# Performance work log

Measured on AMD Instinct MI355X. Metric: run time of the kernel, lower is better.

## Reference

```python
import jax, jax.numpy as jnp
import numpy as np

B, T, F_CGM, F_OTH = 128, 288, 16, 64
U, H = 256, 4
HD = U // H  # head dim 64
EPS = 1e-6
NBLK = 2


def layer_norm(x, s, b):
    m = jnp.mean(x, axis=-1, keepdims=True)
    v = jnp.mean(jnp.square(x - m), axis=-1, keepdims=True)
    return (x - m) * jax.lax.rsqrt(v + EPS) * s + b


def gru(x, Wi, bi, Wh, bhn):
    # flax GRUCell math (deterministic / no dropout):
    # r = sigmoid(W_ir x + b_ir + W_hr h); z = sigmoid(W_iz x + b_iz + W_hz h)
    # n = tanh(W_in x + b_in + r * (W_hn h + b_hn)); h' = (1-z)*n + z*h
    xg = jnp.einsum('btf,fg->btg', x, Wi) + bi  # [B,T,3U], precomputed input gates
    h0 = jnp.zeros((x.shape[0], U), x.dtype)

    def step(h, xg_t):
        hg = h @ Wh  # [B,3U]
        r = jax.nn.sigmoid(xg_t[:, :U] + hg[:, :U])
        z = jax.nn.sigmoid(xg_t[:, U:2 * U] + hg[:, U:2 * U])
        n = jnp.tanh(xg_t[:, 2 * U:] + r * (hg[:, 2 * U:] + bhn))
        h_new = (1.0 - z) * n + z * h
        return h_new, h_new

    _, ys = jax.lax.scan(step, h0, xg.transpose(1, 0, 2))  # time-major scan
    return ys.transpose(1, 0, 2)  # [B,T,U]


def mha(x, Wq, bq, Wk, bk, Wv, bv, Wo, bo):
    b, t, _ = x.shape
    q = (x @ Wq + bq).reshape(b, t, H, HD)
    k = (x @ Wk + bk).reshape(b, t, H, HD)
    v = (x @ Wv + bv).reshape(b, t, H, HD)
    scores = jnp.einsum('bqhd,bkhd->bhqk', q, k) / jnp.sqrt(jnp.asarray(HD, x.dtype))
    p = jax.nn.softmax(scores, axis=-1)
    o = jnp.einsum('bhqk,bkhd->bqhd', p, v).reshape(b, t, U)
    return o @ Wo + bo


def forward(cgm, other, d0_W, d0_b, ln0_s, ln0_b,
            gru_Wi, gru_bi, gru_Wh, gru_bhn, ln1_s, ln1_b,
            Wq, bq, Wk, bk, Wv, bv, Wo, bo, ln2_s, ln2_b,
            m1_W, m1_b, lm1_s, lm1_b, m2_W, m2_b, lm2_s, lm2_b,
            out_W, out_b):
    x = cgm @ d0_W + d0_b                      # [B,T,U]
    x = layer_norm(x, ln0_s, ln0_b)
    for i in range(NBLK):
        skip1 = x
        g = gru(x, gru_Wi[i], gru_bi[i], gru_Wh[i], gru_bhn[i])
        g = layer_norm(g, ln1_s[i], ln1_b[i])
        x = g + skip1                          # dims always match (U == U)
        skip2 = x
        a = mha(x, Wq[i], bq[i], Wk[i], bk[i], Wv[i], bv[i], Wo[i], bo[i])
        x = layer_norm(a + skip2, ln2_s[i], ln2_b[i])
    x = jnp.mean(x, axis=1)                    # [B,U]
    c = jnp.concatenate([x, other], axis=-1)   # [B,U+F_OTH]
    # MLP head; residual branches never match (320->128, 128->64), so no skips
    h1 = layer_norm(jax.nn.relu(c @ m1_W + m1_b), lm1_s, lm1_b)
    h2 = layer_norm(jax.nn.relu(h1 @ m2_W + m2_b), lm2_s, lm2_b)
    return h2 @ out_W + out_b                  # [B,1]


def setup_inputs() -> dict:
    key = jax.random.key(0)
    ks = jax.random.split(key, 16)
    f32 = jnp.float32
    rn = lambda k, shp, s: jax.random.normal(k, shp, dtype=f32) * s
    return {
        'cgm': jax.random.normal(ks[0], (B, T, F_CGM), dtype=f32),
        'other': jax.random.normal(ks[1], (B, F_OTH), dtype=f32),
        'd0_W': rn(ks[2], (F_CGM, U), 0.1), 'd0_b': jnp.zeros((U,), f32),
        'ln0_s': jnp.ones((U,), f32), 'ln0_b': jnp.zeros((U,), f32),
        'gru_Wi': rn(ks[3], (NBLK, U, 3 * U), 0.05), 'gru_bi': jnp.zeros((NBLK, 3 * U), f32),
        'gru_Wh': rn(ks[4], (NBLK, U, 3 * U), 0.05), 'gru_bhn': jnp.zeros((NBLK, U), f32),
        'ln1_s': jnp.ones((NBLK, U), f32), 'ln1_b': jnp.zeros((NBLK, U), f32),
        'Wq': rn(ks[5], (NBLK, U, U), 0.05), 'bq': jnp.zeros((NBLK, U), f32),
        'Wk': rn(ks[6], (NBLK, U, U), 0.05), 'bk': jnp.zeros((NBLK, U), f32),
        'Wv': rn(ks[7], (NBLK, U, U), 0.05), 'bv': jnp.zeros((NBLK, U), f32),
        'Wo': rn(ks[8], (NBLK, U, U), 0.05), 'bo': jnp.zeros((NBLK, U), f32),
        'ln2_s': jnp.ones((NBLK, U), f32), 'ln2_b': jnp.zeros((NBLK, U), f32),
        'm1_W': rn(ks[9], (U + F_OTH, 128), 0.05), 'm1_b': jnp.zeros((128,), f32),
        'lm1_s': jnp.ones((128,), f32), 'lm1_b': jnp.zeros((128,), f32),
        'm2_W': rn(ks[10], (128, 64), 0.05), 'm2_b': jnp.zeros((64,), f32),
        'lm2_s': jnp.ones((64,), f32), 'lm2_b': jnp.zeros((64,), f32),
        'out_W': rn(ks[11], (64, 1), 0.05), 'out_b': jnp.zeros((1,), f32),
    }


def reference(cgm, other, d0_W, d0_b, ln0_s, ln0_b,
              gru_Wi, gru_bi, gru_Wh, gru_bhn, ln1_s, ln1_b,
              Wq, bq, Wk, bk, Wv, bv, Wo, bo, ln2_s, ln2_b,
              m1_W, m1_b, lm1_s, lm1_b, m2_W, m2_b, lm2_s, lm2_b,
              out_W, out_b):
    return forward(cgm, other, d0_W, d0_b, ln0_s, ln0_b,
                   gru_Wi, gru_bi, gru_Wh, gru_bhn, ln1_s, ln1_b,
                   Wq, bq, Wk, bk, Wv, bv, Wo, bo, ln2_s, ln2_b,
                   m1_W, m1_b, lm1_s, lm1_b, m2_W, m2_b, lm2_s, lm2_b,
                   out_W, out_b)
```

## Files before the change

kernel.cpp:

```cpp
#include <hip/hip_runtime.h>
#include <math.h>

#define B_   128
#define T_   288
#define U_   256
#define H_   4
#define HD_  64
#define MT   (B_*T_)
#define EPSF 1e-6f

typedef _Float16 h2_t  __attribute__((ext_vector_type(2)));
typedef _Float16 f16x4 __attribute__((ext_vector_type(4)));
typedef _Float16 f16x8 __attribute__((ext_vector_type(8)));
typedef float    f32x4 __attribute__((ext_vector_type(4)));

#if defined(__has_builtin)
#  if __has_builtin(__builtin_amdgcn_fdot2)
#    define HAS_FDOT2 1
#  endif
#endif
#ifndef HAS_FDOT2
#  define HAS_FDOT2 0
#endif

template<bool TB>
__global__ __launch_bounds__(256) void gemm_kernel(
    const float* __restrict__ A, const float* __restrict__ Bm,
    float* __restrict__ C, const float* __restrict__ bias,
    int M, int N, int K, int lda, int ldb, int ldc,
    long sA1, long sA2, long sB1, long sB2, long sC1, long sC2,
    int zdiv, float alpha)
{
  int z  = blockIdx.z;
  int z1 = z / zdiv, z2 = z - z1 * zdiv;
  A  += (long)z1*sA1 + (long)z2*sA2;
  Bm += (long)z1*sB1 + (long)z2*sB2;
  C  += (long)z1*sC1 + (long)z2*sC2;

  __shared__ float As[16][68];
  __shared__ float Bs[16][68];

  const int tid = threadIdx.x;
  const int tx  = tid & 15;
  const int ty  = tid >> 4;
  const int rowBase = blockIdx.y * 64;
  const int colBase = blockIdx.x * 64;

  float acc[4][4] = {};

  const int lr = tid >> 2;
  const int lk = (tid & 3) << 2;

  for (int k0 = 0; k0 < K; k0 += 16) {
    {
      float4 a4 = {0.f,0.f,0.f,0.f};
      int ar = rowBase + lr;
      if (ar < M) a4 = *(const float4*)(A + (long)ar*lda + k0 + lk);
      As[lk+0][lr]=a4.x; As[lk+1][lr]=a4.y; As[lk+2][lr]=a4.z; As[lk+3][lr]=a4.w;
    }
    if (TB) {
      float4 b4 = {0.f,0.f,0.f,0.f};
      int bn = colBase + lr;
      if (bn < N) b4 = *(const float4*)(Bm + (long)bn*ldb + k0 + lk);
      Bs[lk+0][lr]=b4.x; Bs[lk+1][lr]=b4.y; Bs[lk+2][lr]=b4.z; Bs[lk+3][lr]=b4.w;
    } else {
      int bk  = tid >> 4;
      int bn4 = (tid & 15) << 2;
      float4 b4 = {0.f,0.f,0.f,0.f};
      if (colBase + bn4 < N) b4 = *(const float4*)(Bm + (long)(k0+bk)*ldb + colBase + bn4);
      *(float4*)(&Bs[bk][bn4]) = b4;
    }
    __syncthreads();
    #pragma unroll
    for (int k = 0; k < 16; ++k) {
      float4 av = *(const float4*)(&As[k][ty<<2]);
      float4 bv = *(const float4*)(&Bs[k][tx<<2]);
      acc[0][0]+=av.x*bv.x; acc[0][1]+=av.x*bv.y; acc[0][2]+=av.x*bv.z; acc[0][3]+=av.x*bv.w;
      acc[1][0]+=av.y*bv.x; acc[1][1]+=av.y*bv.y; acc[1][2]+=av.y*bv.z; acc[1][3]+=av.y*bv.w;
      acc[2][0]+=av.z*bv.x; acc[2][1]+=av.z*bv.y; acc[2][2]+=av.z*bv.z; acc[2][3]+=av.z*bv.w;
      acc[3][0]+=av.w*bv.x; acc[3][1]+=av.w*bv.y; acc[3][2]+=av.w*bv.z; acc[3][3]+=av.w*bv.w;
    }
    __syncthreads();
  }

  const int cn = colBase + (tx << 2);
  if (cn < N) {
    float4 bb = {0.f,0.f,0.f,0.f};
    if (bias) bb = *(const float4*)(bias + cn);
    #pragma unroll
    for (int i = 0; i < 4; ++i) {
      int r = rowBase + (ty << 2) + i;
      if (r < M) {
        float4 v;
        v.x = acc[i][0]*alpha + bb.x;
        v.y = acc[i][1]*alpha + bb.y;
        v.z = acc[i][2]*alpha + bb.z;
        v.w = acc[i][3]*alpha + bb.w;
        *(float4*)(C + (long)r*ldc + cn) = v;
      }
    }
  }
}

template<bool OUT16>
__global__ __launch_bounds__(256) void gemm16_kernel(
    const _Float16* __restrict__ A, const _Float16* __restrict__ Bt,
    void* __restrict__ Cv, const float* __restrict__ bias,
    int M, int N, int K, int lda, int ldb, int ldc,
    long sA1, long sA2, long sB1, long sB2, long sC1, long sC2,
    int zdiv, float alpha)
{
  const int z  = blockIdx.z;
  const int z1 = z / zdiv, z2 = z - z1 * zdiv;
  A  += (long)z1*sA1 + (long)z2*sA2;
  Bt += (long)z1*sB1 + (long)z2*sB2;
  float*    Cf = (float*)Cv    + ((long)z1*sC1 + (long)z2*sC2);
  _Float16* Ch = (_Float16*)Cv + ((long)z1*sC1 + (long)z2*sC2);

  __shared__ __align__(16) _Float16 Asf[64][40];
  __shared__ __align__(16) _Float16 Bsf[64][40];
  const int tid  = threadIdx.x;
  const int wv   = tid >> 6;
  const int mw   = wv >> 1, nw = wv & 1;
  const int lane = tid & 63, l16 = lane & 15, lq = lane >> 4;
  const int m0 = blockIdx.y * 64, n0 = blockIdx.x * 64;
  const int srow = tid >> 2, sk = (tid & 3) * 8;

  f32x4 acc00 = {0,0,0,0}, acc01 = {0,0,0,0};
  f32x4 acc10 = {0,0,0,0}, acc11 = {0,0,0,0};

  const long arow = (long)(m0 + srow)*lda + sk;
  const long brow = (long)(n0 + srow)*ldb + sk;

  for (int k0 = 0; k0 < K; k0 += 32) {
    *(f16x8*)&Asf[srow][sk] = *(const f16x8*)&A[arow + k0];
    *(f16x8*)&Bsf[srow][sk] = *(const f16x8*)&Bt[brow + k0];
    __syncthreads();
    f16x8 a0 = *(const f16x8*)&Asf[mw*32 +      l16][lq*8];
    f16x8 a1 = *(const f16x8*)&Asf[mw*32 + 16 + l16][lq*8];
    f16x8 b0 = *(const f16x8*)&Bsf[nw*32 +      l16][lq*8];
    f16x8 b1 = *(const f16x8*)&Bsf[nw*32 + 16 + l16][lq*8];
    acc00 = __builtin_amdgcn_mfma_f32_16x16x32_f16(a0, b0, acc00, 0, 0, 0);
    acc01 = __builtin_amdgcn_mfma_f32_16x16x32_f16(a0, b1, acc01, 0, 0, 0);
    acc10 = __builtin_amdgcn_mfma_f32_16x16x32_f16(a1, b0, acc10, 0, 0, 0);
    acc11 = __builtin_amdgcn_mfma_f32_16x16x32_f16(a1, b1, acc11, 0, 0, 0);
    __syncthreads();
  }

  const int rowb = m0 + mw*32 + lq*4;
#define EPI(ACC, MT_, NT_) { \
    const int col = n0 + nw*32 + (NT_)*16 + l16; \
    if (col < N) { \
      const float bb = bias ? bias[col] : 0.f; \
      const int rb = rowb + (MT_)*16; \
      _Pragma("unroll") \
      for (int i = 0; i < 4; ++i) { \
        if (rb + i < M) { \
          const float val = ACC[i]*alpha + bb; \
          if (OUT16) Ch[(long)(rb+i)*ldc + col] = (_Float16)val; \
          else       Cf[(long)(rb+i)*ldc + col] = val; \
        } } } }
  EPI(acc00,0,0) EPI(acc01,0,1) EPI(acc10,1,0) EPI(acc11,1,1)
#undef EPI
}

__global__ __launch_bounds__(256) void fused_attn_kernel(
    const _Float16* __restrict__ qkv16,
    const _Float16* __restrict__ vt16,
    _Float16* __restrict__ o16)
{
  __shared__ __align__(16) _Float16 Pl[4][16][296];
  const int tid  = threadIdx.x;
  const int w    = tid >> 6;
  const int lane = tid & 63, l16 = lane & 15, lq = lane >> 4;
  const int z = blockIdx.y;
  const int b = z >> 2, h = z & 3;
  const int q0 = blockIdx.x * 64 + w * 16;
  const long rowbase = (long)b * T_;

  const _Float16* qp = qkv16 + (rowbase + q0 + l16) * 768 + h*64 + lq*8;
  f16x8 qf0 = *(const f16x8*)qp;
  f16x8 qf1 = *(const f16x8*)(qp + 32);
  f32x4 acc[18];
  const _Float16* kp = qkv16 + (rowbase + l16) * 768 + 256 + h*64 + lq*8;
  #pragma unroll
  for (int t = 0; t < 18; ++t) {
    f16x8 kf0 = *(const f16x8*)(kp + (long)t*16*768);
    f16x8 kf1 = *(const f16x8*)(kp + (long)t*16*768 + 32);
    f32x4 a = {0.f, 0.f, 0.f, 0.f};
    a = __builtin_amdgcn_mfma_f32_16x16x32_f16(qf0, kf0, a, 0, 0, 0);
    a = __builtin_amdgcn_mfma_f32_16x16x32_f16(qf1, kf1, a, 0, 0, 0);
    acc[t] = a;
  }

  #pragma unroll
  for (int r = 0; r < 4; ++r) {
    float m = -1e30f;
    #pragma unroll
    for (int t = 0; t < 18; ++t) m = fmaxf(m, acc[t][r]);
    m = fmaxf(m, __shfl_xor(m, 1)); m = fmaxf(m, __shfl_xor(m, 2));
    m = fmaxf(m, __shfl_xor(m, 4)); m = fmaxf(m, __shfl_xor(m, 8));
    float p[18];
    float s = 0.f;
    #pragma unroll
    for (int t = 0; t < 18; ++t) {
      p[t] = __expf(0.125f * (acc[t][r] - m));
      s += p[t];
    }
    s += __shfl_xor(s, 1); s += __shfl_xor(s, 2);
    s += __shfl_xor(s, 4); s += __shfl_xor(s, 8);
    const float inv = 1.f / s;
    #pragma unroll
    for (int t = 0; t < 18; ++t)
      Pl[w][lq*4 + r][t*16 + l16] = (_Float16)(p[t] * inv);
  }
  __syncthreads();

  f32x4 accO[4] = {{0,0,0,0},{0,0,0,0},{0,0,0,0},{0,0,0,0}};
  const _Float16* vb = vt16 + ((long)z*64 + l16)*288 + lq*8;
  #pragma unroll
  for (int ks = 0; ks < 9; ++ks) {
    f16x8 pa = *(const f16x8*)&Pl[w][l16][ks*32 + lq*8];
    #pragma unroll
    for (int n = 0; n < 4; ++n) {
      f16x8 vf = *(const f16x8*)(vb + (long)n*16*288 + ks*32);
      accO[n] = __builtin_amdgcn_mfma_f32_16x16x32_f16(pa, vf, accO[n], 0, 0, 0);
    }
  }

  #pragma unroll
  for (int n = 0; n < 4; ++n) {
    const int col = h*64 + n*16 + l16;
    #pragma unroll
    for (int r = 0; r < 4; ++r) {
      const int row = q0 + lq*4 + r;
      if (row < T_)
        o16[(rowbase + row)*256 + col] = (_Float16)accO[n][r];
    }
  }
}

__global__ __launch_bounds__(256) void tpack_kernel(
    const float* __restrict__ src, _Float16* __restrict__ dst, int K, int N)
{
  __shared__ float t[32][33];
  const int tx = threadIdx.x & 31, ty = threadIdx.x >> 5;
  const int n0 = blockIdx.x * 32, k0 = blockIdx.y * 32;
  #pragma unroll
  for (int i = 0; i < 4; ++i)
    t[ty + 8*i][tx] = src[(long)(k0 + ty + 8*i)*N + n0 + tx];
  __syncthreads();
  #pragma unroll
  for (int i = 0; i < 4; ++i)
    dst[(long)(n0 + ty + 8*i)*K + k0 + tx] = (_Float16)t[tx][ty + 8*i];
}

__global__ __launch_bounds__(256) void vtpack_kernel(
    const _Float16* __restrict__ qkv16, _Float16* __restrict__ vt16)
{
  __shared__ _Float16 tile[64][80];
  const int z  = blockIdx.y;
  const int t0 = blockIdx.x * 64;
  const int tr = threadIdx.x >> 2, c4 = (threadIdx.x & 3) * 16;
  const int t  = t0 + tr;
  f16x8 z8 = {};
  const _Float16* src = qkv16 + ((long)((z >> 2)*T_ + t))*768 + 512 + (z & 3)*64 + c4;
  f16x8 v0 = (t < T_) ? *(const f16x8*)src       : z8;
  f16x8 v1 = (t < T_) ? *(const f16x8*)(src + 8) : z8;
  *(f16x8*)&tile[tr][c4]     = v0;
  *(f16x8*)&tile[tr][c4 + 8] = v1;
  __syncthreads();
  _Float16* dst = vt16 + ((long)z*64 + tr)*288 + t0 + c4;
  #pragma unroll
  for (int i = 0; i < 16; ++i)
    if (t0 + c4 + i < T_) dst[i] = tile[c4 + i][tr];
}

__global__ __launch_bounds__(256) void packb_kernel(
    const float* __restrict__ bq, const float* __restrict__ bk,
    const float* __restrict__ bv, float* __restrict__ bp)
{
  int t = threadIdx.x;
  bp[t] = bq[t]; bp[256 + t] = bk[t]; bp[512 + t] = bv[t];
}

__global__ __launch_bounds__(256) void ln256_kernel(
    const float* __restrict__ in, const float* __restrict__ skip_pre,
    const float* __restrict__ skip_post,
    const float* __restrict__ s, const float* __restrict__ b,
    float* __restrict__ out, _Float16* __restrict__ out16)
{
  const int wid  = threadIdx.x >> 6;
  const int lane = threadIdx.x & 63;
  const long row  = (long)blockIdx.x * 4 + wid;
  const long base = row * 256 + lane * 4;

  float4 v = *(const float4*)(in + base);
  if (skip_pre) {
    float4 sp = *(const float4*)(skip_pre + base);
    v.x += sp.x; v.y += sp.y; v.z += sp.z; v.w += sp.w;
  }
  float m = v.x + v.y + v.z + v.w;
  for (int o = 32; o; o >>= 1) m += __shfl_xor(m, o);
  m *= (1.f/256.f);
  float4 d = { v.x - m, v.y - m, v.z - m, v.w - m };
  float var = d.x*d.x + d.y*d.y + d.z*d.z + d.w*d.w;
  for (int o = 32; o; o >>= 1) var += __shfl_xor(var, o);
  var *= (1.f/256.f);
  const float inv = rsqrtf(var + EPSF);
  float4 sv = *(const float4*)(s + lane*4);
  float4 bv = *(const float4*)(b + lane*4);
  float4 y;
  y.x = d.x*inv*sv.x + bv.x;
  y.y = d.y*inv*sv.y + bv.y;
  y.z = d.z*inv*sv.z + bv.z;
  y.w = d.w*inv*sv.w + bv.w;
  if (skip_post) {
    float4 sp = *(const float4*)(skip_post + base);
    y.x += sp.x; y.y += sp.y; y.z += sp.z; y.w += sp.w;
  }
  *(float4*)(out + base) = y;
  if (out16) {
    f16x4 o16 = {(_Float16)y.x, (_Float16)y.y, (_Float16)y.z, (_Float16)y.w};
    *(f16x4*)(out16 + base) = o16;
  }
}

__global__ __launch_bounds__(1024, 1) void gru_scan_kernel(
    const float* __restrict__ xg,
    const float* __restrict__ Wh,
    const float* __restrict__ bhn,
    float* __restrict__ g)
{
  const int b   = blockIdx.x;
  const int tid = threadIdx.x;
  const int u   = tid & 255;
  const int kq  = tid >> 8;

  __shared__ float hf[256];
  __shared__ __align__(16) h2_t hh2s[128];
  __shared__ float part[4][3][256];

  h2_t wr[32], wz[32], wn[32];
  #pragma unroll
  for (int r = 0; r < 32; ++r) {
    const float* p0 = Wh + (long)(kq*64 + 2*r)*768 + u;
    const float* p1 = p0 + 768;
    h2_t a; a.x = (_Float16)p0[0];   a.y = (_Float16)p1[0];   wr[r] = a;
    h2_t c; c.x = (_Float16)p0[256]; c.y = (_Float16)p1[256]; wz[r] = c;
    h2_t d; d.x = (_Float16)p0[512]; d.y = (_Float16)p1[512]; wn[r] = d;
  }
  float bn = (kq == 0) ? bhn[u] : 0.f;
  if (tid < 256) hf[tid] = 0.f;
  if (tid < 128) { h2_t zz; zz.x = (_Float16)0.f; zz.y = (_Float16)0.f; hh2s[tid] = zz; }
  __syncthreads();

  const float* xgb = xg + (long)b*T_*768;
  float* gb = g + (long)b*T_*256;

  for (int t = 0; t < T_; ++t) {
    float xr = 0.f, xz = 0.f, xn = 0.f;
    if (kq == 0) {
      const float* xt = xgb + (long)t*768;
      xr = xt[u]; xz = xt[u+256]; xn = xt[u+512];
    }
    const float4* hq4 = (const float4*)(&hh2s[kq*32]);
    float ar = 0.f, az = 0.f, an = 0.f;
    #pragma unroll
    for (int c = 0; c < 8; ++c) {
      const float4 hc = hq4[c];
      union { float f; h2_t h; } u0, u1, u2, u3;
      u0.f = hc.x; u1.f = hc.y; u2.f = hc.z; u3.f = hc.w;
#if HAS_FDOT2
      ar = __builtin_amdgcn_fdot2(u0.h, wr[c*4+0], ar, false);
      az = __builtin_amdgcn_fdot2(u0.h, wz[c*4+0], az, false);
      an = __builtin_amdgcn_fdot2(u0.h, wn[c*4+0], an, false);
      ar = __builtin_amdgcn_fdot2(u1.h, wr[c*4+1], ar, false);
      az = __builtin_amdgcn_fdot2(u1.h, wz[c*4+1], az, false);
      an = __builtin_amdgcn_fdot2(u1.h, wn[c*4+1], an, false);
      ar = __builtin_amdgcn_fdot2(u2.h, wr[c*4+2], ar, false);
      az = __builtin_amdgcn_fdot2(u2.h, wz[c*4+2], az, false);
      an = __builtin_amdgcn_fdot2(u2.h, wn[c*4+2], an, false);
      ar = __builtin_amdgcn_fdot2(u3.h, wr[c*4+3], ar, false);
      az = __builtin_amdgcn_fdot2(u3.h, wz[c*4+3], az, false);
      an = __builtin_amdgcn_fdot2(u3.h, wn[c*4+3], an, false);
#else
      ar += (float)u0.h.x*(float)wr[c*4+0].x + (float)u0.h.y*(float)wr[c*4+0].y;
      az += (float)u0.h.x*(float)wz[c*4+0].x + (float)u0.h.y*(float)wz[c*4+0].y;
      an += (float)u0.h.x*(float)wn[c*4+0].x + (float)u0.h.y*(float)wn[c*4+0].y;
      ar += (float)u1.h.x*(float)wr[c*4+1].x + (float)u1.h.y*(float)wr[c*4+1].y;
      az += (float)u1.h.x*(float)wz[c*4+1].x + (float)u1.h.y*(float)wz[c*4+1].y;
      an += (float)u1.h.x*(float)wn[c*4+1].x + (float)u1.h.y*(float)wn[c*4+1].y;
      ar += (float)u2.h.x*(float)wr[c*4+2].x + (float)u2.h.y*(float)wr[c*4+2].y;
      az += (float)u2.h.x*(float)wz[c*4+2].x + (float)u2.h.y*(float)wz[c*4+2].y;
      an += (float)u2.h.x*(float)wn[c*4+2].x + (float)u2.h.y*(float)wn[c*4+2].y;
      ar += (float)u3.h.x*(float)wr[c*4+3].x + (float)u3.h.y*(float)wr[c*4+3].y;
      az += (float)u3.h.x*(float)wz[c*4+3].x + (float)u3.h.y*(float)wz[c*4+3].y;
      an += (float)u3.h.x*(float)wn[c*4+3].x + (float)u3.h.y*(float)wn[c*4+3].y;
#endif
    }
    part[kq][0][u] = ar; part[kq][1][u] = az; part[kq][2][u] = an;
    __syncthreads();
    if (kq == 0) {
      float hr = part[0][0][u]+part[1][0][u]+part[2][0][u]+part[3][0][u] + xr;
      float hz = part[0][1][u]+part[1][1][u]+part[2][1][u]+part[3][1][u] + xz;
      float hn = part[0][2][u]+part[1][2][u]+part[2][2][u]+part[3][2][u];
      float rr = 1.f / (1.f + __expf(-hr));
      float z  = 1.f / (1.f + __expf(-hz));
      float nx = xn + rr * (hn + bn);
      float e2 = __expf(2.f * nx);
      float nv = (e2 - 1.f) / (e2 + 1.f);
      float hnew = (1.f - z) * nv + z * hf[u];
      hf[u] = hnew;
      ((_Float16*)hh2s)[u] = (_Float16)hnew;
      gb[(long)t*256 + u] = hnew;
    }
    __syncthreads();
  }
}

__global__ __launch_bounds__(256) void meanT_kernel(
    const float* __restrict__ x, float* __restrict__ xm)
{
  int b = blockIdx.x, u = threadIdx.x;
  const float* p = x + (long)b*T_*U_ + u;
  float s = 0.f;
  for (int t = 0; t < T_; ++t) s += p[(long)t*U_];
  xm[b*U_ + u] = s * (1.f/(float)T_);
}

__global__ __launch_bounds__(128) void head_kernel(
    const float* __restrict__ xm, const float* __restrict__ other,
    const float* __restrict__ m1W, const float* __restrict__ m1b,
    const float* __restrict__ l1s, const float* __restrict__ l1b,
    const float* __restrict__ m2W, const float* __restrict__ m2b,
    const float* __restrict__ l2s, const float* __restrict__ l2b,
    const float* __restrict__ oW,  const float* __restrict__ ob,
    float* __restrict__ outp)
{
  __shared__ float c[320];
  __shared__ float h1[128];
  __shared__ float sb[2];
  int b = blockIdx.x, tid = threadIdx.x;
  c[tid]       = xm[b*256 + tid];
  c[tid + 128] = xm[b*256 + tid + 128];
  if (tid < 64) c[256 + tid] = other[b*64 + tid];
  __syncthreads();
  float s = m1b[tid];
  for (int i = 0; i < 320; ++i) s += c[i] * m1W[i*128 + tid];
  s = fmaxf(s, 0.f);
  float m = s;
  for (int o = 32; o; o >>= 1) m += __shfl_xor(m, o);
  if ((tid & 63) == 0) sb[tid >> 6] = m;
  __syncthreads();
  m = (sb[0] + sb[1]) * (1.f/128.f);
  __syncthreads();
  float d = s - m, var = d*d;
  for (int o = 32; o; o >>= 1) var += __shfl_xor(var, o);
  if ((tid & 63) == 0) sb[tid >> 6] = var;
  __syncthreads();
  var = (sb[0] + sb[1]) * (1.f/128.f);
  h1[tid] = d * rsqrtf(var + EPSF) * l1s[tid] + l1b[tid];
  __syncthreads();
  if (tid < 64) {
    float s2 = m2b[tid];
    for (int i = 0; i < 128; ++i) s2 += h1[i] * m2W[i*64 + tid];
    s2 = fmaxf(s2, 0.f);
    float m2 = s2;
    for (int o = 32; o; o >>= 1) m2 += __shfl_xor(m2, o);
    m2 *= (1.f/64.f);
    float d2 = s2 - m2, v2 = d2*d2;
    for (int o = 32; o; o >>= 1) v2 += __shfl_xor(v2, o);
    v2 *= (1.f/64.f);
    float h2v = d2 * rsqrtf(v2 + EPSF) * l2s[tid] + l2b[tid];
    float y = h2v * oW[tid];
    for (int o = 32; o; o >>= 1) y += __shfl_xor(y, o);
    if (tid == 0) outp[b] = y + ob[0];
  }
}

static inline void gemm_nn(hipStream_t st, const float* A, const float* Bm, float* C,
                           const float* bias, int M, int N, int K,
                           int lda, int ldb, int ldc, float alpha)
{
  dim3 g((N + 63)/64, (M + 63)/64, 1);
  gemm_kernel<false><<<g, 256, 0, st>>>(A, Bm, C, bias, M, N, K, lda, ldb, ldc,
                                        0,0,0,0,0,0, 1, alpha);
}

static inline void gemm16(hipStream_t st, const _Float16* A, const _Float16* Bt,
                          void* C, const float* bias, int M, int N, int K,
                          int ldc, bool out16)
{
  dim3 g((N + 63)/64, (M + 63)/64, 1);
  if (out16)
    gemm16_kernel<true ><<<g, 256, 0, st>>>(A, Bt, C, bias, M, N, K, K, K, ldc,
                                            0,0,0,0,0,0, 1, 1.f);
  else
    gemm16_kernel<false><<<g, 256, 0, st>>>(A, Bt, C, bias, M, N, K, K, K, ldc,
                                            0,0,0,0,0,0, 1, 1.f);
}

extern "C" void kernel_launch(void* const* d_in, const int* in_sizes, int n_in,
                              void* d_out, int out_size, void* d_ws, size_t ws_size,
                              hipStream_t stream)
{
  const float* cgm   = (const float*)d_in[0];
  const float* other = (const float*)d_in[1];
  const float* d0_W  = (const float*)d_in[2];
  const float* d0_b  = (const float*)d_in[3];
  const float* ln0_s = (const float*)d_in[4];
  const float* ln0_b = (const float*)d_in[5];
  const float* gWi   = (const float*)d_in[6];
  const float* gbi   = (const float*)d_in[7];
  const float* gWh   = (const float*)d_in[8];
  const float* gbhn  = (const float*)d_in[9];
  const float* ln1_s = (const float*)d_in[10];
  const float* ln1_b = (const float*)d_in[11];
  const float* Wq    = (const float*)d_in[12];
  const float* bq    = (const float*)d_in[13];
  const float* Wk    = (const float*)d_in[14];
  const float* bk    = (const float*)d_in[15];
  const float* Wv    = (const float*)d_in[16];
  const float* bv    = (const float*)d_in[17];
  const float* Wo    = (const float*)d_in[18];
  const float* bo    = (const float*)d_in[19];
  const float* ln2_s = (const float*)d_in[20];
  const float* ln2_b = (const float*)d_in[21];
  const float* m1W   = (const float*)d_in[22];
  const float* m1b   = (const float*)d_in[23];
  const float* l1s   = (const float*)d_in[24];
  const float* l1b   = (const float*)d_in[25];
  const float* m2W   = (const float*)d_in[26];
  const float* m2b   = (const float*)d_in[27];
  const float* l2s   = (const float*)d_in[28];
  const float* l2b   = (const float*)d_in[29];
  const float* oW    = (const float*)d_in[30];
  const float* ob    = (const float*)d_in[31];
  float* out = (float*)d_out;

  float* ws   = (float*)d_ws;
  float* big  = ws;
  float* x    = big  + 28311552;
  float* go   = x    +  9437184;
  float* Sbuf = go   +  9437184;
  (void)in_sizes; (void)n_in; (void)out_size; (void)ws_size;

  _Float16* a16   = (_Float16*)Sbuf;
  _Float16* qkv16 = (_Float16*)big;
  _Float16* vt16  = (_Float16*)big + 28311552;
  _Float16* o16   = (_Float16*)go;
  _Float16* wtWi  = (_Float16*)(Sbuf + 4718592);
  _Float16* wtQKV = (_Float16*)(Sbuf + 4718592 + 98304);
  _Float16* wtWo  = (_Float16*)(Sbuf + 4718592 + 196608);
  float*    bqkv  =             Sbuf + 4718592 + 229376;
  float*    xmean =             Sbuf + 4718592 + 230144;

  gemm_nn(stream, cgm, d0_W, big, d0_b, MT, 256, 16, 16, 256, 256, 1.f);
  ln256_kernel<<<MT/4, 256, 0, stream>>>(big, nullptr, nullptr, ln0_s, ln0_b, x, a16);

  for (int i = 0; i < 2; ++i) {
    const float* Wh_i = gWh + (long)i*196608;

    tpack_kernel<<<dim3(24, 8), 256, 0, stream>>>(gWi + (long)i*196608, wtWi, 256, 768);
    gemm16(stream, a16, wtWi, big, gbi + i*768, MT, 768, 256, 768, false);
    gru_scan_kernel<<<128, 1024, 0, stream>>>(big, Wh_i, gbhn + i*256, go);
    ln256_kernel<<<MT/4, 256, 0, stream>>>(go, nullptr, x, ln1_s + i*256, ln1_b + i*256, x, a16);

    tpack_kernel<<<dim3(8, 8), 256, 0, stream>>>(Wq + (long)i*65536, wtQKV,            256, 256);
    tpack_kernel<<<dim3(8, 8), 256, 0, stream>>>(Wk + (long)i*65536, wtQKV + 256*256,  256, 256);
    tpack_kernel<<<dim3(8, 8), 256, 0, stream>>>(Wv + (long)i*65536, wtQKV + 512*256,  256, 256);
    packb_kernel<<<1, 256, 0, stream>>>(bq + i*256, bk + i*256, bv + i*256, bqkv);
    gemm16(stream, a16, wtQKV, qkv16, bqkv, MT, 768, 256, 768, true);

    vtpack_kernel<<<dim3(5, 512), 256, 0, stream>>>(qkv16, vt16);
    fused_attn_kernel<<<dim3(5, 512), 256, 0, stream>>>(qkv16, vt16, o16);

    tpack_kernel<<<dim3(8, 8), 256, 0, stream>>>(Wo + (long)i*65536, wtWo, 256, 256);
    gemm16(stream, o16, wtWo, big, bo + i*256, MT, 256, 256, 256, false);
    ln256_kernel<<<MT/4, 256, 0, stream>>>(big, x, nullptr, ln2_s + i*256, ln2_b + i*256, x, a16);
  }

  meanT_kernel<<<128, 256, 0, stream>>>(x, xmean);
  head_kernel<<<128, 128, 0, stream>>>(xmean, other, m1W, m1b, l1s, l1b,
                                       m2W, m2b, l2s, l2b, oW, ob, out);
}
```

Baseline: 1.460 ms.

## Enlarge fp16 MFMA GEMM tiles to 128x128 and batch weight packing

Replaces the 64x64-tile fp16 MFMA GEMM with a 128x128-tile version where each wave computes a 4x4 grid of 16x16 MFMA tiles. This raises operand reuse from LDS and cuts global reloads for the input-gate, QKV and output projections. All weight transposes and bias packs for both layers are merged into one launch at the start, and the time-mean is folded into the head kernel. The bigger tile uses more registers (launch bound of 2 blocks per CU) and removes the bounds checks, so it relies on M and N being multiples of 128.

```diff
diff --git a/kernel.cpp b/kernel.cpp
--- a/kernel.cpp
+++ b/kernel.cpp
@@ -103,65 +103,65 @@
 }
 
 template<bool OUT16>
-__global__ __launch_bounds__(256) void gemm16_kernel(
+__global__ __launch_bounds__(256, 2) void gemm128_kernel(
     const _Float16* __restrict__ A, const _Float16* __restrict__ Bt,
     void* __restrict__ Cv, const float* __restrict__ bias,
-    int M, int N, int K, int lda, int ldb, int ldc,
-    long sA1, long sA2, long sB1, long sB2, long sC1, long sC2,
-    int zdiv, float alpha)
-{
-  const int z  = blockIdx.z;
-  const int z1 = z / zdiv, z2 = z - z1 * zdiv;
-  A  += (long)z1*sA1 + (long)z2*sA2;
-  Bt += (long)z1*sB1 + (long)z2*sB2;
-  float*    Cf = (float*)Cv    + ((long)z1*sC1 + (long)z2*sC2);
-  _Float16* Ch = (_Float16*)Cv + ((long)z1*sC1 + (long)z2*sC2);
-
-  __shared__ __align__(16) _Float16 Asf[64][40];
-  __shared__ __align__(16) _Float16 Bsf[64][40];
+    int M, int N, int K, int ldc)
+{
+  __shared__ __align__(16) _Float16 Asf[128][40];
+  __shared__ __align__(16) _Float16 Bsf[128][40];
   const int tid  = threadIdx.x;
   const int wv   = tid >> 6;
   const int mw   = wv >> 1, nw = wv & 1;
   const int lane = tid & 63, l16 = lane & 15, lq = lane >> 4;
-  const int m0 = blockIdx.y * 64, n0 = blockIdx.x * 64;
+  const int m0 = blockIdx.y * 128, n0 = blockIdx.x * 128;
   const int srow = tid >> 2, sk = (tid & 3) * 8;
 
-  f32x4 acc00 = {0,0,0,0}, acc01 = {0,0,0,0};
-  f32x4 acc10 = {0,0,0,0}, acc11 = {0,0,0,0};
-
-  const long arow = (long)(m0 + srow)*lda + sk;
-  const long brow = (long)(n0 + srow)*ldb + sk;
+  f32x4 acc[4][4] = {};
+
+  const long arow0 = (long)(m0 + srow)*K + sk;
+  const long arow1 = (long)(m0 + srow + 64)*K + sk;
+  const long brow0 = (long)(n0 + srow)*K + sk;
+  const long brow1 = (long)(n0 + srow + 64)*K + sk;
 
   for (int k0 = 0; k0 < K; k0 += 32) {
-    *(f16x8*)&Asf[srow][sk] = *(const f16x8*)&A[arow + k0];
-    *(f16x8*)&Bsf[srow][sk] = *(const f16x8*)&Bt[brow + k0];
+    *(f16x8*)&Asf[srow     ][sk] = *(const f16x8*)&A[arow0 + k0];
+    *(f16x8*)&Asf[srow + 64][sk] = *(const f16x8*)&A[arow1 + k0];
+    *(f16x8*)&Bsf[srow     ][sk] = *(const f16x8*)&Bt[brow0 + k0];
+    *(f16x8*)&Bsf[srow + 64][sk] = *(const f16x8*)&Bt[brow1 + k0];
     __syncthreads();
-    f16x8 a0 = *(const f16x8*)&Asf[mw*32 +      l16][lq*8];
-    f16x8 a1 = *(const f16x8*)&Asf[mw*32 + 16 + l16][lq*8];
-    f16x8 b0 = *(const f16x8*)&Bsf[nw*32 +      l16][lq*8];
-    f16x8 b1 = *(const f16x8*)&Bsf[nw*32 + 16 + l16][lq*8];
-    acc00 = __builtin_amdgcn_mfma_f32_16x16x32_f16(a0, b0, acc00, 0, 0, 0);
-    acc01 = __builtin_amdgcn_mfma_f32_16x16x32_f16(a0, b1, acc01, 0, 0, 0);
-    acc10 = __builtin_amdgcn_mfma_f32_16x16x32_f16(a1, b0, acc10, 0, 0, 0);
-    acc11 = __builtin_amdgcn_mfma_f32_16x16x32_f16(a1, b1, acc11, 0, 0, 0);
+    f16x8 af[4], bf[4];
+    #pragma unroll
+    for (int mt = 0; mt < 4; ++mt)
+      af[mt] = *(const f16x8*)&Asf[mw*64 + mt*16 + l16][lq*8];
+    #pragma unroll
+    for (int nt = 0; nt < 4; ++nt)
+      bf[nt] = *(const f16x8*)&Bsf[nw*64 + nt*16 + l16][lq*8];
+    #pragma unroll
+    for (int mt = 0; mt < 4; ++mt)
+      #pragma unroll
+      for (int nt = 0; nt < 4; ++nt)
+        acc[mt][nt] = __builtin_amdgcn_mfma_f32_16x16x32_f16(af[mt], bf[nt], acc[mt][nt], 0, 0, 0);
     __syncthreads();
   }
 
-  const int rowb = m0 + mw*32 + lq*4;
-#define EPI(ACC, MT_, NT_) { \
-    const int col = n0 + nw*32 + (NT_)*16 + l16; \
-    if (col < N) { \
-      const float bb = bias ? bias[col] : 0.f; \
-      const int rb = rowb + (MT_)*16; \
-      _Pragma("unroll") \
-      for (int i = 0; i < 4; ++i) { \
-        if (rb + i < M) { \
-          const float val = ACC[i]*alpha + bb; \
-          if (OUT16) Ch[(long)(rb+i)*ldc + col] = (_Float16)val; \
-          else       Cf[(long)(rb+i)*ldc + col] = val; \
-        } } } }
-  EPI(acc00,0,0) EPI(acc01,0,1) EPI(acc10,1,0) EPI(acc11,1,1)
-#undef EPI
+  float*    Cf = (float*)Cv;
+  _Float16* Ch = (_Float16*)Cv;
+  #pragma unroll
+  for (int nt = 0; nt < 4; ++nt) {
+    const int col = n0 + nw*64 + nt*16 + l16;
+    const float bb = bias ? bias[col] : 0.f;
+    #pragma unroll
+    for (int mt = 0; mt < 4; ++mt) {
+      const int rb = m0 + mw*64 + mt*16 + lq*4;
+      #pragma unroll
+      for (int i = 0; i < 4; ++i) {
+        const float val = acc[mt][nt][i] + bb;
+        if (OUT16) Ch[(long)(rb+i)*ldc + col] = (_Float16)val;
+        else       Cf[(long)(rb+i)*ldc + col] = val;
+      }
+    }
+  }
 }
 
 __global__ __launch_bounds__(256) void fused_attn_kernel(
@@ -240,19 +240,43 @@
   }
 }
 
-__global__ __launch_bounds__(256) void tpack_kernel(
-    const float* __restrict__ src, _Float16* __restrict__ dst, int K, int N)
-{
+__global__ __launch_bounds__(256) void packall_kernel(
+    const float* __restrict__ gWi, const float* __restrict__ Wq,
+    const float* __restrict__ Wk,  const float* __restrict__ Wv,
+    const float* __restrict__ Wo,  const float* __restrict__ bq,
+    const float* __restrict__ bk,  const float* __restrict__ bv,
+    _Float16* __restrict__ wtWi, _Float16* __restrict__ wtQKV,
+    _Float16* __restrict__ wtWo, float* __restrict__ bqkv)
+{
+  const int z = blockIdx.z;
+  if (z >= 10) {
+    if (blockIdx.x || blockIdx.y) return;
+    const int li = z - 10, t = threadIdx.x;
+    bqkv[li*768 + t]       = bq[li*256 + t];
+    bqkv[li*768 + 256 + t] = bk[li*256 + t];
+    bqkv[li*768 + 512 + t] = bv[li*256 + t];
+    return;
+  }
+  const int i = z / 5, m = z - i*5;
+  const float* src; _Float16* dst; int N;
+  if (m == 0)      { src = gWi + (long)i*196608; dst = wtWi  + (long)i*196608; N = 768; }
+  else if (m == 4) { src = Wo  + (long)i*65536;  dst = wtWo  + (long)i*65536;  N = 256; }
+  else {
+    const float* s3 = (m == 1) ? Wq : (m == 2) ? Wk : Wv;
+    src = s3 + (long)i*65536; dst = wtQKV + (long)i*196608 + (long)(m-1)*65536; N = 256;
+  }
+  const int n0 = blockIdx.x * 32, k0 = blockIdx.y * 32;
+  if (n0 >= N) return;
+
   __shared__ float t[32][33];
   const int tx = threadIdx.x & 31, ty = threadIdx.x >> 5;
-  const int n0 = blockIdx.x * 32, k0 = blockIdx.y * 32;
-  #pragma unroll
-  for (int i = 0; i < 4; ++i)
-    t[ty + 8*i][tx] = src[(long)(k0 + ty + 8*i)*N + n0 + tx];
-  __syncthreads();
-  #pragma unroll
-  for (int i = 0; i < 4; ++i)
-    dst[(long)(n0 + ty + 8*i)*K + k0 + tx] = (_Float16)t[tx][ty + 8*i];
+  #pragma unroll
+  for (int j = 0; j < 4; ++j)
+    t[ty + 8*j][tx] = src[(long)(k0 + ty + 8*j)*N + n0 + tx];
+  __syncthreads();
+  #pragma unroll
+  for (int j = 0; j < 4; ++j)
+    dst[(long)(n0 + ty + 8*j)*256 + k0 + tx] = (_Float16)t[tx][ty + 8*j];
 }
 
 __global__ __launch_bounds__(256) void vtpack_kernel(
@@ -274,14 +298,6 @@
   #pragma unroll
   for (int i = 0; i < 16; ++i)
     if (t0 + c4 + i < T_) dst[i] = tile[c4 + i][tr];
-}
-
-__global__ __launch_bounds__(256) void packb_kernel(
-    const float* __restrict__ bq, const float* __restrict__ bk,
-    const float* __restrict__ bv, float* __restrict__ bp)
-{
-  int t = threadIdx.x;
-  bp[t] = bq[t]; bp[256 + t] = bk[t]; bp[512 + t] = bv[t];
 }
 
 __global__ __launch_bounds__(256) void ln256_kernel(
@@ -419,18 +435,8 @@
   }
 }
 
-__global__ __launch_bounds__(256) void meanT_kernel(
-    const float* __restrict__ x, float* __restrict__ xm)
-{
-  int b = blockIdx.x, u = threadIdx.x;
-  const float* p = x + (long)b*T_*U_ + u;
-  float s = 0.f;
-  for (int t = 0; t < T_; ++t) s += p[(long)t*U_];
-  xm[b*U_ + u] = s * (1.f/(float)T_);
-}
-
 __global__ __launch_bounds__(128) void head_kernel(
-    const float* __restrict__ xm, const float* __restrict__ other,
+    const float* __restrict__ x, const float* __restrict__ other,
     const float* __restrict__ m1W, const float* __restrict__ m1b,
     const float* __restrict__ l1s, const float* __restrict__ l1b,
     const float* __restrict__ m2W, const float* __restrict__ m2b,
@@ -442,8 +448,16 @@
   __shared__ float h1[128];
   __shared__ float sb[2];
   int b = blockIdx.x, tid = threadIdx.x;
-  c[tid]       = xm[b*256 + tid];
-  c[tid + 128] = xm[b*256 + tid + 128];
+  {
+    const float* xb = x + (long)b*T_*256;
+    float s0 = 0.f, s1 = 0.f;
+    for (int t = 0; t < T_; ++t) {
+      s0 += xb[(long)t*256 + tid];
+      s1 += xb[(long)t*256 + tid + 128];
+    }
+    c[tid]       = s0 * (1.f/(float)T_);
+    c[tid + 128] = s1 * (1.f/(float)T_);
+  }
   if (tid < 64) c[256 + tid] = other[b*64 + tid];
   __syncthreads();
   float s = m1b[tid];
@@ -486,19 +500,6 @@
   dim3 g((N + 63)/64, (M + 63)/64, 1);
   gemm_kernel<false><<<g, 256, 0, st>>>(A, Bm, C, bias, M, N, K, lda, ldb, ldc,
                                         0,0,0,0,0,0, 1, alpha);
-}
-
-static inline void gemm16(hipStream_t st, const _Float16* A, const _Float16* Bt,
-                          void* C, const float* bias, int M, int N, int K,
-                          int ldc, bool out16)
-{
-  dim3 g((N + 63)/64, (M + 63)/64, 1);
-  if (out16)
-    gemm16_kernel<true ><<<g, 256, 0, st>>>(A, Bt, C, bias, M, N, K, K, K, ldc,
-                                            0,0,0,0,0,0, 1, 1.f);
-  else
-    gemm16_kernel<false><<<g, 256, 0, st>>>(A, Bt, C, bias, M, N, K, K, K, ldc,
-                                            0,0,0,0,0,0, 1, 1.f);
 }
 
 extern "C" void kernel_launch(void* const* d_in, const int* in_sizes, int n_in,
@@ -546,15 +547,18 @@
   float* Sbuf = go   +  9437184;
   (void)in_sizes; (void)n_in; (void)out_size; (void)ws_size;
 
-  _Float16* a16   = (_Float16*)Sbuf;
+  _Float16* h0    = (_Float16*)Sbuf;
+  _Float16* a16   = h0;
+  _Float16* wtWi  = h0 + 9437184;
+  _Float16* wtQKV = h0 + 9830400;
+  _Float16* wtWo  = h0 + 10223616;
+  float*    bqkv  = Sbuf + 5177344;
   _Float16* qkv16 = (_Float16*)big;
   _Float16* vt16  = (_Float16*)big + 28311552;
   _Float16* o16   = (_Float16*)go;
-  _Float16* wtWi  = (_Float16*)(Sbuf + 4718592);
-  _Float16* wtQKV = (_Float16*)(Sbuf + 4718592 + 98304);
-  _Float16* wtWo  = (_Float16*)(Sbuf + 4718592 + 196608);
-  float*    bqkv  =             Sbuf + 4718592 + 229376;
-  float*    xmean =             Sbuf + 4718592 + 230144;
+
+  packall_kernel<<<dim3(24, 8, 12), 256, 0, stream>>>(
+      gWi, Wq, Wk, Wv, Wo, bq, bk, bv, wtWi, wtQKV, wtWo, bqkv);
 
   gemm_nn(stream, cgm, d0_W, big, d0_b, MT, 256, 16, 16, 256, 256, 1.f);
   ln256_kernel<<<MT/4, 256, 0, stream>>>(big, nullptr, nullptr, ln0_s, ln0_b, x, a16);
@@ -562,26 +566,22 @@
   for (int i = 0; i < 2; ++i) {
     const float* Wh_i = gWh + (long)i*196608;
 
-    tpack_kernel<<<dim3(24, 8), 256, 0, stream>>>(gWi + (long)i*196608, wtWi, 256, 768);
-    gemm16(stream, a16, wtWi, big, gbi + i*768, MT, 768, 256, 768, false);
+    gemm128_kernel<false><<<dim3(6, 288), 256, 0, stream>>>(
+        a16, wtWi + (long)i*196608, big, gbi + i*768, MT, 768, 256, 768);
     gru_scan_kernel<<<128, 1024, 0, stream>>>(big, Wh_i, gbhn + i*256, go);
     ln256_kernel<<<MT/4, 256, 0, stream>>>(go, nullptr, x, ln1_s + i*256, ln1_b + i*256, x, a16);
 
-    tpack_kernel<<<dim3(8, 8), 256, 0, stream>>>(Wq + (long)i*65536, wtQKV,            256, 256);
-    tpack_kernel<<<dim3(8, 8), 256, 0, stream>>>(Wk + (long)i*65536, wtQKV + 256*256,  256, 256);
-    tpack_kernel<<<dim3(8, 8), 256, 0, stream>>>(Wv + (long)i*65536, wtQKV + 512*256,  256, 256);
-    packb_kernel<<<1, 256, 0, stream>>>(bq + i*256, bk + i*256, bv + i*256, bqkv);
-    gemm16(stream, a16, wtQKV, qkv16, bqkv, MT, 768, 256, 768, true);
+    gemm128_kernel<true><<<dim3(6, 288), 256, 0, stream>>>(
+        a16, wtQKV + (long)i*196608, qkv16, bqkv + i*768, MT, 768, 256, 768);
 
     vtpack_kernel<<<dim3(5, 512), 256, 0, stream>>>(qkv16, vt16);
     fused_attn_kernel<<<dim3(5, 512), 256, 0, stream>>>(qkv16, vt16, o16);
 
-    tpack_kernel<<<dim3(8, 8), 256, 0, stream>>>(Wo + (long)i*65536, wtWo, 256, 256);
-    gemm16(stream, o16, wtWo, big, bo + i*256, MT, 256, 256, 256, false);
+    gemm128_kernel<false><<<dim3(2, 288), 256, 0, stream>>>(
+        o16, wtWo + (long)i*65536, big, bo + i*256, MT, 256, 256, 256);
     ln256_kernel<<<MT/4, 256, 0, stream>>>(big, x, nullptr, ln2_s + i*256, ln2_b + i*256, x, a16);
   }
 
-  meanT_kernel<<<128, 256, 0, stream>>>(x, xmean);
-  head_kernel<<<128, 128, 0, stream>>>(xmean, other, m1W, m1b, l1s, l1b,
+  head_kernel<<<128, 128, 0, stream>>>(x, other, m1W, m1b, l1s, l1b,
                                        m2W, m2b, l2s, l2b, oW, ob, out);
 }
```

After: 1.391 ms. -4.7%, faster.
